# Kernel optimization log

Hardware: AMD Instinct MI355X
Metric: run time of the kernel (lower is better)

## Reference

```python
import jax, jax.numpy as jnp
import numpy as np

D_MODEL = 1024
N_HEADS = 16
SCALES = (1, 2)
D_K = D_MODEL // N_HEADS          # 64
HPS = N_HEADS // len(SCALES)      # heads per scale = 8


def _upsample_linear(x, target_len):
    """PyTorch F.interpolate(mode='linear', align_corners=False) along dim 2.
    x: [b, h, l, d] -> [b, h, target_len, d]"""
    b, h, l, d = x.shape
    if l == target_len:
        return x
    # source coordinates, clamped at 0 like PyTorch's area_pixel_compute_source_index
    coords = (jnp.arange(target_len, dtype=jnp.float32) + 0.5) * (l / target_len) - 0.5
    coords = jnp.maximum(coords, 0.0)
    i0 = jnp.clip(jnp.floor(coords).astype(jnp.int32), 0, l - 1)
    i1 = jnp.minimum(i0 + 1, l - 1)
    w = (coords - i0.astype(jnp.float32))[None, None, :, None]
    return x[:, :, i0, :] * (1.0 - w) + x[:, :, i1, :] * w


def setup_inputs() -> dict:
    rng = jax.random.key(0)
    ks = jax.random.split(rng, 7)
    B, S = 2, 2048
    s = 1.0 / np.sqrt(D_MODEL)
    mkw = lambda k: jax.random.normal(k, (D_MODEL, D_MODEL), jnp.float32) * s
    zb = jnp.zeros((D_MODEL,), jnp.float32)
    return {
        "query": jax.random.normal(ks[0], (B, S, D_MODEL), jnp.float32),
        "key": jax.random.normal(ks[1], (B, S, D_MODEL), jnp.float32),
        "value": jax.random.normal(ks[2], (B, S, D_MODEL), jnp.float32),
        "w_q": mkw(ks[3]), "b_q": zb,
        "w_k": mkw(ks[4]), "b_k": zb,
        "w_v": mkw(ks[5]), "b_v": zb,
        "w_o": mkw(ks[6]), "b_o": zb,
    }


def reference(query, key, value, w_q, b_q, w_k, b_k, w_v, b_v, w_o, b_o):
    B, S, _ = query.shape
    inv_scale = 1.0 / np.sqrt(D_K).astype(np.float32)

    def proj(x, W, b):
        # [B,S,D] -> [B,H,S,dk]
        return (x @ W + b).reshape(B, S, N_HEADS, D_K).transpose(0, 2, 1, 3)

    Q = proj(query, w_q, b_q)
    K = proj(key, w_k, b_k)
    V = proj(value, w_v, b_v)

    outs = []
    for i, f in enumerate(SCALES):
        hs = slice(i * HPS, (i + 1) * HPS)
        Qd = Q[:, hs, ::f]                      # strided downsample along seq
        Kd = K[:, hs, ::f]
        Vd = V[:, hs, ::f]
        scores = jnp.einsum('bhqd,bhkd->bhqk', Qd, Kd) * inv_scale
        attn = jax.nn.softmax(scores, axis=-1)   # dropout inactive (eval)
        o = jnp.einsum('bhqk,bhkd->bhqd', attn, Vd)
        outs.append(_upsample_linear(o, S))

    out = jnp.concatenate(outs, axis=1)          # [B,H,S,dk]
    out = out.transpose(0, 2, 1, 3).reshape(B, S, D_MODEL)
    return out @ w_o + b_o
```

## Files before the change

kernel.cpp:

```cpp
#include <hip/hip_runtime.h>
#include <hip/hip_bf16.h>
#include <cstddef>

#define DMODEL 1024
#define DK 64
#define S1 2048
#define S2 1024
#define NBATCH 2
#define NSPLIT 2
#define KVTILE 64
#define QSCALE 0.1803368801111244f

typedef __bf16 bf16x8 __attribute__((ext_vector_type(8)));
typedef float f32x4 __attribute__((ext_vector_type(4)));
typedef unsigned short u16x4 __attribute__((ext_vector_type(4)));
typedef unsigned int u32x4 __attribute__((ext_vector_type(4)));

__device__ __forceinline__ unsigned short f2bf(float f) {
  unsigned u = __builtin_bit_cast(unsigned, f);
  u = (u + 0x7FFFu + ((u >> 16) & 1u)) >> 16;
  return (unsigned short)u;
}
__device__ __forceinline__ float bf2f(unsigned short u) {
  unsigned x = ((unsigned)u) << 16;
  return __builtin_bit_cast(float, x);
}
__device__ __forceinline__ unsigned cvt_pk_bf16(float a, float b) {
  unsigned r;
  asm("v_cvt_pk_bf16_f32 %0, %1, %2" : "=v"(r) : "v"(a), "v"(b));
  return r;
}
__device__ __forceinline__ bf16x8 ld_bf16x8(const unsigned short* p) {
  u32x4 v = *reinterpret_cast<const u32x4*>(p);
  return __builtin_bit_cast(bf16x8, v);
}
__device__ __forceinline__ void gload_lds16(const void* g, void* l) {
  __builtin_amdgcn_global_load_lds(
      (const __attribute__((address_space(1))) unsigned*)g,
      (__attribute__((address_space(3))) unsigned*)l, 16, 0, 0);
}
__device__ __forceinline__ bf16x8 ld_tile(const unsigned short* tile, int row, int cbytes) {
  const char* p = (const char*)tile + row * 128 + (cbytes ^ ((row & 7) << 4));
  return ld_bf16x8((const unsigned short*)p);
}

__global__ __launch_bounds__(256) void cvt_bf16_kernel(
    const float* __restrict__ in, unsigned short* __restrict__ out, int n4) {
  int i = blockIdx.x * 256 + threadIdx.x;
  if (i >= n4) return;
  f32x4 v = reinterpret_cast<const f32x4*>(in)[i];
  u16x4 r;
#pragma unroll
  for (int j = 0; j < 4; ++j) r[j] = f2bf(v[j]);
  reinterpret_cast<u16x4*>(out)[i] = r;
}

__global__ __launch_bounds__(1024) void transpose_w_kernel(
    const float* __restrict__ W, unsigned short* __restrict__ Wt) {
  __shared__ float t[32][33];
  int tx = threadIdx.x, ty = threadIdx.y;
  int n = blockIdx.x * 32 + tx;
  int k = blockIdx.y * 32 + ty;
  t[ty][tx] = W[(size_t)k * DMODEL + n];
  __syncthreads();
  int n2 = blockIdx.x * 32 + ty;
  int k2 = blockIdx.y * 32 + tx;
  Wt[(size_t)n2 * DMODEL + k2] = f2bf(t[tx][ty]);
}

template <int MODE>
__global__ __launch_bounds__(256) void gemm_bf16(
    const unsigned short* __restrict__ A, const unsigned short* __restrict__ Bt,
    const float* __restrict__ bias, float sc, float* __restrict__ outF,
    unsigned short* __restrict__ out1, unsigned short* __restrict__ out2) {
  __shared__ __align__(16) unsigned short As[2][128 * 64];
  __shared__ __align__(16) unsigned short Bs[2][64 * 64];
  int w = threadIdx.x >> 6, lane = threadIdx.x & 63;
  int lo = lane & 15, hi = lane >> 4;
  int rowBase = blockIdx.y * 128;
  int colBase = blockIdx.x * 64;
  int rl = lane >> 3;
  int ck = lane & 7;

  auto stageA = [&](int buf, int k0) {
#pragma unroll
    for (int i = 0; i < 4; ++i) {
      int slot = w * 4 + i;
      int rloc = slot * 8 + rl;
      int cb = (ck * 16) ^ ((rloc & 7) << 4);
      const char* g = (const char*)(A + (size_t)(rowBase + rloc) * DMODEL + k0) + cb;
      gload_lds16(g, (void*)&As[buf][slot * 512]);
    }
  };
  auto stageB = [&](int buf, int k0) {
#pragma unroll
    for (int i = 0; i < 2; ++i) {
      int slot = w * 2 + i;
      int rloc = slot * 8 + rl;
      int cb = (ck * 16) ^ ((rloc & 7) << 4);
      const char* g = (const char*)(Bt + (size_t)(colBase + rloc) * DMODEL + k0) + cb;
      gload_lds16(g, (void*)&Bs[buf][slot * 512]);
    }
  };

  f32x4 acc[2][4] = {};

  stageA(0, 0);
  stageB(0, 0);
  __syncthreads();

  const int NT = DMODEL / 64;
  for (int t = 0; t < NT; ++t) {
    int buf = t & 1;
    if (t + 1 < NT) {
      stageA(buf ^ 1, (t + 1) * 64);
      stageB(buf ^ 1, (t + 1) * 64);
    }
    bf16x8 af[2][2], bfr[4][2];
#pragma unroll
    for (int mt = 0; mt < 2; ++mt)
#pragma unroll
      for (int kk = 0; kk < 2; ++kk)
        af[mt][kk] = ld_tile(&As[buf][0], w * 32 + mt * 16 + lo, kk * 64 + hi * 16);
#pragma unroll
    for (int nt = 0; nt < 4; ++nt)
#pragma unroll
      for (int kk = 0; kk < 2; ++kk)
        bfr[nt][kk] = ld_tile(&Bs[buf][0], nt * 16 + lo, kk * 64 + hi * 16);
#pragma unroll
    for (int kk = 0; kk < 2; ++kk)
#pragma unroll
      for (int mt = 0; mt < 2; ++mt)
#pragma unroll
        for (int nt = 0; nt < 4; ++nt)
          acc[mt][nt] = __builtin_amdgcn_mfma_f32_16x16x32_bf16(
              af[mt][kk], bfr[nt][kk], acc[mt][nt], 0, 0, 0);
    __syncthreads();
  }

#pragma unroll
  for (int mt = 0; mt < 2; ++mt) {
#pragma unroll
    for (int nt = 0; nt < 4; ++nt) {
      int col = colBase + nt * 16 + lo;
      float bv = bias[col];
#pragma unroll
      for (int r = 0; r < 4; ++r) {
        int row = rowBase + w * 32 + mt * 16 + hi * 4 + r;
        float v = (acc[mt][nt][r] + bv) * sc;
        if (MODE == 0) {
          outF[(size_t)row * DMODEL + col] = v;
        } else {
          int b = row >> 11, s = row & 2047;
          int h = col >> 6, d = col & 63;
          if (MODE == 1) {
            if (h < 8)
              out1[(((size_t)(b * 8 + h)) * S1 + s) * DK + d] = f2bf(v);
            else if (!(s & 1))
              out2[(((size_t)(b * 8 + (h - 8))) * S2 + (s >> 1)) * DK + d] = f2bf(v);
          } else {
            if (h < 8)
              out1[(((size_t)(b * 8 + h)) * DK + d) * S1 + s] = f2bf(v);
            else if (!(s & 1))
              out2[(((size_t)(b * 8 + (h - 8))) * DK + d) * S2 + (s >> 1)] = f2bf(v);
          }
        }
      }
    }
  }
}

__global__ __launch_bounds__(256) void attn_kernel(
    const unsigned short* __restrict__ Q, const unsigned short* __restrict__ K,
    const unsigned short* __restrict__ Vt, float* __restrict__ Opart,
    float* __restrict__ ml, int Sq, int Skv) {
  __shared__ __align__(16) unsigned short KV[2][2][64 * 64];
  __shared__ __align__(16) unsigned P_lds[4][16][36];
  int w = threadIdx.x >> 6, lane = threadIdx.x & 63;
  int lo = lane & 15, hi = lane >> 4;
  int bh = blockIdx.z;
  int split = blockIdx.y;
  int q0 = blockIdx.x * 64 + w * 16;
  int splitLen = Skv / NSPLIT;
  int kvbase = split * splitLen;
  int nIter = splitLen / KVTILE;

  const unsigned short* Qp = Q + ((size_t)bh * Sq + q0) * DK;
  bf16x8 qb0 = ld_bf16x8(Qp + lo * DK + hi * 8);
  bf16x8 qb1 = ld_bf16x8(Qp + lo * DK + 32 + hi * 8);

  const unsigned short* Kb = K + (size_t)bh * Skv * DK;
  const unsigned short* Vb = Vt + (size_t)bh * DK * Skv;

  auto stage = [&](int buf, int kv0) {
    int rl = lane >> 3;
    int cbl = (lane & 7) * 16;
#pragma unroll
    for (int i = 0; i < 2; ++i) {
      int rt = w * 16 + i * 8 + rl;
      int gcb = cbl ^ ((rt & 7) << 4);
      const char* gK = (const char*)(Kb + (size_t)(kv0 + rt) * DK) + gcb;
      gload_lds16(gK, (void*)&KV[buf][0][(w * 16 + i * 8) * 64]);
      const char* gV = (const char*)(Vb + (size_t)rt * Skv + kv0) + gcb;
      gload_lds16(gV, (void*)&KV[buf][1][(w * 16 + i * 8) * 64]);
    }
  };

  float m = -1e30f, l = 0.f;
  f32x4 oacc[4] = {};

  stage(0, kvbase);
  __syncthreads();

  for (int it = 0; it < nIter; ++it) {
    if (it + 1 < nIter) stage((it + 1) & 1, kvbase + (it + 1) * KVTILE);

    const unsigned short* Kt = &KV[it & 1][0][0];
    const unsigned short* Vtl = &KV[it & 1][1][0];

    f32x4 s[4];
#pragma unroll
    for (int t = 0; t < 4; ++t) {
      bf16x8 ka0 = ld_tile(Kt, t * 16 + lo, hi * 16);
      bf16x8 ka1 = ld_tile(Kt, t * 16 + lo, 64 + hi * 16);
      f32x4 z = {};
      z = __builtin_amdgcn_mfma_f32_16x16x32_bf16(ka0, qb0, z, 0, 0, 0);
      s[t] = __builtin_amdgcn_mfma_f32_16x16x32_bf16(ka1, qb1, z, 0, 0, 0);
    }

    float x[16];
#pragma unroll
    for (int t = 0; t < 4; ++t)
#pragma unroll
      for (int r = 0; r < 4; ++r) x[t * 4 + r] = s[t][r];
    float tmax = x[0];
#pragma unroll
    for (int j = 1; j < 16; ++j) tmax = fmaxf(tmax, x[j]);
    tmax = fmaxf(tmax, __shfl_xor(tmax, 16));
    tmax = fmaxf(tmax, __shfl_xor(tmax, 32));

    if (!__all(tmax - m <= 8.0f)) {
      float mnew = fmaxf(m, tmax);
      float alpha = exp2f(m - mnew);
      m = mnew;
      l *= alpha;
      float ar[4];
#pragma unroll
      for (int r = 0; r < 4; ++r) ar[r] = __shfl(alpha, hi * 4 + r);
#pragma unroll
      for (int nb = 0; nb < 4; ++nb) {
        f32x4 t = oacc[nb];
        t[0] *= ar[0];
        t[1] *= ar[1];
        t[2] *= ar[2];
        t[3] *= ar[3];
        oacc[nb] = t;
      }
    }

    float tsum = 0.f;
#pragma unroll
    for (int j = 0; j < 16; ++j) {
      x[j] = exp2f(x[j] - m);
      tsum += x[j];
    }
    tsum += __shfl_xor(tsum, 16);
    tsum += __shfl_xor(tsum, 32);
    l += tsum;

    unsigned* prow = &P_lds[w][lo][0];
#pragma unroll
    for (int t = 0; t < 4; ++t) {
      uint2 pk;
      pk.x = cvt_pk_bf16(x[t * 4 + 0], x[t * 4 + 1]);
      pk.y = cvt_pk_bf16(x[t * 4 + 2], x[t * 4 + 3]);
      *reinterpret_cast<uint2*>(prow + t * 8 + 2 * hi) = pk;
    }

    bf16x8 pa0 = ld_bf16x8(reinterpret_cast<unsigned short*>(prow + 4 * hi));
    bf16x8 pa1 = ld_bf16x8(reinterpret_cast<unsigned short*>(prow + 16 + 4 * hi));
#pragma unroll
    for (int nb = 0; nb < 4; ++nb) {
      bf16x8 vb0 = ld_tile(Vtl, nb * 16 + lo, hi * 16);
      bf16x8 vb1 = ld_tile(Vtl, nb * 16 + lo, 64 + hi * 16);
      oacc[nb] = __builtin_amdgcn_mfma_f32_16x16x32_bf16(pa0, vb0, oacc[nb], 0, 0, 0);
      oacc[nb] = __builtin_amdgcn_mfma_f32_16x16x32_bf16(pa1, vb1, oacc[nb], 0, 0, 0);
    }

    __syncthreads();
  }

  float* Op = Opart + (((size_t)(split * 16 + bh)) * Sq + q0) * DK;
#pragma unroll
  for (int nb = 0; nb < 4; ++nb)
#pragma unroll
    for (int r = 0; r < 4; ++r)
      Op[(size_t)(hi * 4 + r) * DK + nb * 16 + lo] = oacc[nb][r];
  if (hi == 0) {
    float2* mlp = reinterpret_cast<float2*>(ml) + ((size_t)(split * 16 + bh)) * Sq + q0 + lo;
    *mlp = make_float2(m, l);
  }
}

template <int MODE>
__global__ __launch_bounds__(256) void combine_kernel(
    const float* __restrict__ Opart, const float* __restrict__ ml,
    unsigned short* __restrict__ out, int Sq) {
  int rr = blockIdx.x * 4 + (threadIdx.x >> 6);
  int d = threadIdx.x & 63;
  int bh = rr / Sq, q = rr - bh * Sq;
  const float2* mlp = reinterpret_cast<const float2*>(ml);
  float2 ml0 = mlp[(size_t)bh * Sq + q];
  float2 ml1 = mlp[(size_t)(16 + bh) * Sq + q];
  float M = fmaxf(ml0.x, ml1.x);
  float w0 = exp2f(ml0.x - M), w1 = exp2f(ml1.x - M);
  float inv = 1.0f / (ml0.y * w0 + ml1.y * w1);
  float o0 = Opart[((size_t)bh * Sq + q) * DK + d];
  float o1 = Opart[((size_t)(16 + bh) * Sq + q) * DK + d];
  float v = (o0 * w0 + o1 * w1) * inv;
  if (MODE == 1) {
    int b = bh >> 3, h = bh & 7;
    out[((size_t)(b * S1 + q)) * DMODEL + h * 64 + d] = f2bf(v);
  } else {
    out[((size_t)bh * Sq + q) * DK + d] = f2bf(v);
  }
}

__global__ __launch_bounds__(256) void upsample_kernel(
    const unsigned short* __restrict__ O2, unsigned short* __restrict__ ctx) {
  int c = blockIdx.x * 256 + threadIdx.x;
  if (c >= NBATCH * S1 * 512) return;
  int col = c & 511;
  int m_ = c >> 9;
  int s = m_ & (S1 - 1);
  int b = m_ >> 11;
  int h = col >> 6, d = col & 63;
  const unsigned short* X = O2 + ((size_t)(b * 8 + h)) * S2 * DK + d;
  int mm = s >> 1;
  float v;
  if (s & 1) {
    int i1 = (mm + 1 < S2) ? mm + 1 : S2 - 1;
    v = 0.75f * bf2f(X[(size_t)mm * DK]) + 0.25f * bf2f(X[(size_t)i1 * DK]);
  } else {
    v = (mm == 0) ? bf2f(X[0])
                  : (0.25f * bf2f(X[(size_t)(mm - 1) * DK]) +
                     0.75f * bf2f(X[(size_t)mm * DK]));
  }
  ctx[((size_t)(b * S1 + s)) * DMODEL + 512 + col] = f2bf(v);
}

extern "C" void kernel_launch(void* const* d_in, const int* in_sizes, int n_in,
                              void* d_out, int out_size, void* d_ws, size_t ws_size,
                              hipStream_t stream) {
  const float* query = (const float*)d_in[0];
  const float* key = (const float*)d_in[1];
  const float* value = (const float*)d_in[2];
  const float* w_q = (const float*)d_in[3];
  const float* b_q = (const float*)d_in[4];
  const float* w_k = (const float*)d_in[5];
  const float* b_k = (const float*)d_in[6];
  const float* w_v = (const float*)d_in[7];
  const float* b_v = (const float*)d_in[8];
  const float* w_o = (const float*)d_in[9];
  const float* b_o = (const float*)d_in[10];
  float* out = (float*)d_out;

  char* ws = (char*)d_ws;
  size_t off = 0;
  auto alloc = [&](size_t bytes) {
    char* p = ws + off;
    off += (bytes + 255) & ~(size_t)255;
    return p;
  };
  const size_t WT_B = (size_t)DMODEL * DMODEL * 2;
  unsigned short* WqT = (unsigned short*)alloc(WT_B);
  unsigned short* WkT = (unsigned short*)alloc(WT_B);
  unsigned short* WvT = (unsigned short*)alloc(WT_B);
  unsigned short* WoT = (unsigned short*)alloc(WT_B);
  unsigned short* xk = (unsigned short*)alloc((size_t)NBATCH * S1 * DMODEL * 2);
  unsigned short* xv = (unsigned short*)alloc((size_t)NBATCH * S1 * DMODEL * 2);
  float* Opart1 = (float*)xk;
  unsigned short* Q1 = (unsigned short*)alloc((size_t)16 * S1 * DK * 2);
  unsigned short* K1 = (unsigned short*)alloc((size_t)16 * S1 * DK * 2);
  unsigned short* V1t = (unsigned short*)alloc((size_t)16 * S1 * DK * 2);
  unsigned short* Q2 = (unsigned short*)alloc((size_t)16 * S2 * DK * 2);
  unsigned short* K2 = (unsigned short*)alloc((size_t)16 * S2 * DK * 2);
  unsigned short* V2t = (unsigned short*)alloc((size_t)16 * S2 * DK * 2);
  unsigned short* O2 = (unsigned short*)alloc((size_t)16 * S2 * DK * 2);
  unsigned short* ctx = (unsigned short*)alloc((size_t)NBATCH * S1 * DMODEL * 2);
  unsigned short* xq = ctx;
  float* Opart2 = (float*)alloc((size_t)NSPLIT * 16 * S2 * DK * 4);
  float* ml1 = (float*)alloc((size_t)NSPLIT * 16 * S1 * 2 * 4);
  float* ml2 = (float*)alloc((size_t)NSPLIT * 16 * S2 * 2 * 4);

  const int n4 = NBATCH * S1 * DMODEL / 4;
  cvt_bf16_kernel<<<n4 / 256, 256, 0, stream>>>(query, xq, n4);
  cvt_bf16_kernel<<<n4 / 256, 256, 0, stream>>>(key, xk, n4);
  cvt_bf16_kernel<<<n4 / 256, 256, 0, stream>>>(value, xv, n4);

  dim3 tb(32, 32), tg(32, 32);
  transpose_w_kernel<<<tg, tb, 0, stream>>>(w_q, WqT);
  transpose_w_kernel<<<tg, tb, 0, stream>>>(w_k, WkT);
  transpose_w_kernel<<<tg, tb, 0, stream>>>(w_v, WvT);
  transpose_w_kernel<<<tg, tb, 0, stream>>>(w_o, WoT);

  dim3 gg(DMODEL / 64, (NBATCH * S1) / 128);
  gemm_bf16<1><<<gg, 256, 0, stream>>>(xq, WqT, b_q, QSCALE, nullptr, Q1, Q2);
  gemm_bf16<1><<<gg, 256, 0, stream>>>(xk, WkT, b_k, 1.0f, nullptr, K1, K2);
  gemm_bf16<2><<<gg, 256, 0, stream>>>(xv, WvT, b_v, 1.0f, nullptr, V1t, V2t);

  attn_kernel<<<dim3(S1 / 64, NSPLIT, 16), 256, 0, stream>>>(Q1, K1, V1t, Opart1, ml1, S1, S1);
  attn_kernel<<<dim3(S2 / 64, NSPLIT, 16), 256, 0, stream>>>(Q2, K2, V2t, Opart2, ml2, S2, S2);

  combine_kernel<1><<<(16 * S1) / 4, 256, 0, stream>>>(Opart1, ml1, ctx, S1);
  combine_kernel<0><<<(16 * S2) / 4, 256, 0, stream>>>(Opart2, ml2, O2, S2);

  upsample_kernel<<<(NBATCH * S1 * 512) / 256, 256, 0, stream>>>(O2, ctx);

  gemm_bf16<0><<<gg, 256, 0, stream>>>(ctx, WoT, b_o, 1.0f, out, nullptr, nullptr);
}
```

Measured before the change: 298.5 us.

## Process two 16-row query tiles per wave to reuse K/V fragments

Each wave now handles 32 query rows as two 16-row sub-tiles, so every K and V fragment read from shared memory feeds twice as many MFMAs. The block covers 128 queries and the grid is halved. LDS tile addresses are precomputed once per wave (row offset and swizzle) instead of per load. This cuts LDS traffic and global K/V staging per query, at the cost of more registers and fewer blocks, which may reduce occupancy and parallelism on the smaller scale-2 attention.

Result: no change. 296.7 us (-0.6%).

```diff
diff --git a/kernel.cpp b/kernel.cpp
--- a/kernel.cpp
+++ b/kernel.cpp
@@ -42,6 +42,9 @@
 __device__ __forceinline__ bf16x8 ld_tile(const unsigned short* tile, int row, int cbytes) {
   const char* p = (const char*)tile + row * 128 + (cbytes ^ ((row & 7) << 4));
   return ld_bf16x8((const unsigned short*)p);
+}
+__device__ __forceinline__ bf16x8 ld_off(const void* base, int byteoff) {
+  return ld_bf16x8((const unsigned short*)((const char*)base + byteoff));
 }
 
 __global__ __launch_bounds__(256) void cvt_bf16_kernel(
@@ -175,19 +178,21 @@
     const unsigned short* __restrict__ Vt, float* __restrict__ Opart,
     float* __restrict__ ml, int Sq, int Skv) {
   __shared__ __align__(16) unsigned short KV[2][2][64 * 64];
-  __shared__ __align__(16) unsigned P_lds[4][16][36];
+  __shared__ __align__(16) unsigned P_lds[4][2][16][36];
   int w = threadIdx.x >> 6, lane = threadIdx.x & 63;
   int lo = lane & 15, hi = lane >> 4;
   int bh = blockIdx.z;
   int split = blockIdx.y;
-  int q0 = blockIdx.x * 64 + w * 16;
+  int q0 = blockIdx.x * 128 + w * 32;
   int splitLen = Skv / NSPLIT;
   int kvbase = split * splitLen;
   int nIter = splitLen / KVTILE;
 
   const unsigned short* Qp = Q + ((size_t)bh * Sq + q0) * DK;
-  bf16x8 qb0 = ld_bf16x8(Qp + lo * DK + hi * 8);
-  bf16x8 qb1 = ld_bf16x8(Qp + lo * DK + 32 + hi * 8);
+  bf16x8 qA0 = ld_bf16x8(Qp + lo * DK + hi * 8);
+  bf16x8 qA1 = ld_bf16x8(Qp + lo * DK + 32 + hi * 8);
+  bf16x8 qB0 = ld_bf16x8(Qp + (16 + lo) * DK + hi * 8);
+  bf16x8 qB1 = ld_bf16x8(Qp + (16 + lo) * DK + 32 + hi * 8);
 
   const unsigned short* Kb = K + (size_t)bh * Skv * DK;
   const unsigned short* Vb = Vt + (size_t)bh * DK * Skv;
@@ -206,8 +211,13 @@
     }
   };
 
-  float m = -1e30f, l = 0.f;
-  f32x4 oacc[4] = {};
+  int rowoff = lo * 128;
+  int sw = (lo & 7) << 4;
+  int colz0 = (hi * 16) ^ sw;
+  int colz1 = (64 + hi * 16) ^ sw;
+
+  float mA = -1e30f, lA = 0.f, mB = -1e30f, lB = 0.f;
+  f32x4 oaccA[4] = {}, oaccB[4] = {};
 
   stage(0, kvbase);
   __syncthreads();
@@ -215,90 +225,108 @@
   for (int it = 0; it < nIter; ++it) {
     if (it + 1 < nIter) stage((it + 1) & 1, kvbase + (it + 1) * KVTILE);
 
-    const unsigned short* Kt = &KV[it & 1][0][0];
-    const unsigned short* Vtl = &KV[it & 1][1][0];
-
-    f32x4 s[4];
+    const char* Kt = (const char*)&KV[it & 1][0][0];
+    const char* Vtl = (const char*)&KV[it & 1][1][0];
+
+    f32x4 sA[4], sB[4];
 #pragma unroll
     for (int t = 0; t < 4; ++t) {
-      bf16x8 ka0 = ld_tile(Kt, t * 16 + lo, hi * 16);
-      bf16x8 ka1 = ld_tile(Kt, t * 16 + lo, 64 + hi * 16);
-      f32x4 z = {};
-      z = __builtin_amdgcn_mfma_f32_16x16x32_bf16(ka0, qb0, z, 0, 0, 0);
-      s[t] = __builtin_amdgcn_mfma_f32_16x16x32_bf16(ka1, qb1, z, 0, 0, 0);
-    }
-
-    float x[16];
-#pragma unroll
-    for (int t = 0; t < 4; ++t)
-#pragma unroll
-      for (int r = 0; r < 4; ++r) x[t * 4 + r] = s[t][r];
-    float tmax = x[0];
-#pragma unroll
-    for (int j = 1; j < 16; ++j) tmax = fmaxf(tmax, x[j]);
-    tmax = fmaxf(tmax, __shfl_xor(tmax, 16));
-    tmax = fmaxf(tmax, __shfl_xor(tmax, 32));
-
-    if (!__all(tmax - m <= 8.0f)) {
-      float mnew = fmaxf(m, tmax);
-      float alpha = exp2f(m - mnew);
-      m = mnew;
-      l *= alpha;
-      float ar[4];
-#pragma unroll
-      for (int r = 0; r < 4; ++r) ar[r] = __shfl(alpha, hi * 4 + r);
-#pragma unroll
-      for (int nb = 0; nb < 4; ++nb) {
-        f32x4 t = oacc[nb];
-        t[0] *= ar[0];
-        t[1] *= ar[1];
-        t[2] *= ar[2];
-        t[3] *= ar[3];
-        oacc[nb] = t;
+      bf16x8 ka0 = ld_off(Kt, t * 2048 + rowoff + colz0);
+      bf16x8 ka1 = ld_off(Kt, t * 2048 + rowoff + colz1);
+      f32x4 zA = {};
+      zA = __builtin_amdgcn_mfma_f32_16x16x32_bf16(ka0, qA0, zA, 0, 0, 0);
+      sA[t] = __builtin_amdgcn_mfma_f32_16x16x32_bf16(ka1, qA1, zA, 0, 0, 0);
+      f32x4 zB = {};
+      zB = __builtin_amdgcn_mfma_f32_16x16x32_bf16(ka0, qB0, zB, 0, 0, 0);
+      sB[t] = __builtin_amdgcn_mfma_f32_16x16x32_bf16(ka1, qB1, zB, 0, 0, 0);
+    }
+
+#pragma unroll
+    for (int tile = 0; tile < 2; ++tile) {
+      f32x4* s = tile ? sB : sA;
+      float& m = tile ? mB : mA;
+      float& l = tile ? lB : lA;
+      f32x4* oacc = tile ? oaccB : oaccA;
+
+      float t01 = fmaxf(fmaxf(s[0][0], s[0][1]), fmaxf(s[0][2], s[0][3]));
+      float t23 = fmaxf(fmaxf(s[1][0], s[1][1]), fmaxf(s[1][2], s[1][3]));
+      float t45 = fmaxf(fmaxf(s[2][0], s[2][1]), fmaxf(s[2][2], s[2][3]));
+      float t67 = fmaxf(fmaxf(s[3][0], s[3][1]), fmaxf(s[3][2], s[3][3]));
+      float tmax = fmaxf(fmaxf(t01, t23), fmaxf(t45, t67));
+      tmax = fmaxf(tmax, __shfl_xor(tmax, 16));
+      tmax = fmaxf(tmax, __shfl_xor(tmax, 32));
+
+      if (!__all(tmax - m <= 8.0f)) {
+        float mnew = fmaxf(m, tmax);
+        float alpha = exp2f(m - mnew);
+        m = mnew;
+        l *= alpha;
+        float ar[4];
+#pragma unroll
+        for (int r = 0; r < 4; ++r) ar[r] = __shfl(alpha, hi * 4 + r);
+#pragma unroll
+        for (int nb = 0; nb < 4; ++nb) {
+          f32x4 t = oacc[nb];
+          t[0] *= ar[0];
+          t[1] *= ar[1];
+          t[2] *= ar[2];
+          t[3] *= ar[3];
+          oacc[nb] = t;
+        }
       }
-    }
-
-    float tsum = 0.f;
-#pragma unroll
-    for (int j = 0; j < 16; ++j) {
-      x[j] = exp2f(x[j] - m);
-      tsum += x[j];
-    }
-    tsum += __shfl_xor(tsum, 16);
-    tsum += __shfl_xor(tsum, 32);
-    l += tsum;
-
-    unsigned* prow = &P_lds[w][lo][0];
-#pragma unroll
-    for (int t = 0; t < 4; ++t) {
-      uint2 pk;
-      pk.x = cvt_pk_bf16(x[t * 4 + 0], x[t * 4 + 1]);
-      pk.y = cvt_pk_bf16(x[t * 4 + 2], x[t * 4 + 3]);
-      *reinterpret_cast<uint2*>(prow + t * 8 + 2 * hi) = pk;
-    }
-
-    bf16x8 pa0 = ld_bf16x8(reinterpret_cast<unsigned short*>(prow + 4 * hi));
-    bf16x8 pa1 = ld_bf16x8(reinterpret_cast<unsigned short*>(prow + 16 + 4 * hi));
+
+      float tsum = 0.f;
+#pragma unroll
+      for (int t = 0; t < 4; ++t)
+#pragma unroll
+        for (int r = 0; r < 4; ++r) {
+          s[t][r] = exp2f(s[t][r] - m);
+          tsum += s[t][r];
+        }
+      tsum += __shfl_xor(tsum, 16);
+      tsum += __shfl_xor(tsum, 32);
+      l += tsum;
+
+      unsigned* prow = &P_lds[w][tile][lo][0];
+#pragma unroll
+      for (int t = 0; t < 4; ++t) {
+        uint2 pk;
+        pk.x = cvt_pk_bf16(s[t][0], s[t][1]);
+        pk.y = cvt_pk_bf16(s[t][2], s[t][3]);
+        *reinterpret_cast<uint2*>(prow + t * 8 + 2 * hi) = pk;
+      }
+    }
+
+    bf16x8 paA0 = ld_bf16x8((unsigned short*)(&P_lds[w][0][lo][0] + 4 * hi));
+    bf16x8 paA1 = ld_bf16x8((unsigned short*)(&P_lds[w][0][lo][0] + 16 + 4 * hi));
+    bf16x8 paB0 = ld_bf16x8((unsigned short*)(&P_lds[w][1][lo][0] + 4 * hi));
+    bf16x8 paB1 = ld_bf16x8((unsigned short*)(&P_lds[w][1][lo][0] + 16 + 4 * hi));
 #pragma unroll
     for (int nb = 0; nb < 4; ++nb) {
-      bf16x8 vb0 = ld_tile(Vtl, nb * 16 + lo, hi * 16);
-      bf16x8 vb1 = ld_tile(Vtl, nb * 16 + lo, 64 + hi * 16);
-      oacc[nb] = __builtin_amdgcn_mfma_f32_16x16x32_bf16(pa0, vb0, oacc[nb], 0, 0, 0);
-      oacc[nb] = __builtin_amdgcn_mfma_f32_16x16x32_bf16(pa1, vb1, oacc[nb], 0, 0, 0);
+      bf16x8 vb0 = ld_off(Vtl, nb * 2048 + rowoff + colz0);
+      bf16x8 vb1 = ld_off(Vtl, nb * 2048 + rowoff + colz1);
+      oaccA[nb] = __builtin_amdgcn_mfma_f32_16x16x32_bf16(paA0, vb0, oaccA[nb], 0, 0, 0);
+      oaccA[nb] = __builtin_amdgcn_mfma_f32_16x16x32_bf16(paA1, vb1, oaccA[nb], 0, 0, 0);
+      oaccB[nb] = __builtin_amdgcn_mfma_f32_16x16x32_bf16(paB0, vb0, oaccB[nb], 0, 0, 0);
+      oaccB[nb] = __builtin_amdgcn_mfma_f32_16x16x32_bf16(paB1, vb1, oaccB[nb], 0, 0, 0);
     }
 
     __syncthreads();
   }
 
-  float* Op = Opart + (((size_t)(split * 16 + bh)) * Sq + q0) * DK;
+  float* OpA = Opart + (((size_t)(split * 16 + bh)) * Sq + q0) * DK;
+  float* OpB = OpA + (size_t)16 * DK;
 #pragma unroll
   for (int nb = 0; nb < 4; ++nb)
 #pragma unroll
-    for (int r = 0; r < 4; ++r)
-      Op[(size_t)(hi * 4 + r) * DK + nb * 16 + lo] = oacc[nb][r];
+    for (int r = 0; r < 4; ++r) {
+      OpA[(size_t)(hi * 4 + r) * DK + nb * 16 + lo] = oaccA[nb][r];
+      OpB[(size_t)(hi * 4 + r) * DK + nb * 16 + lo] = oaccB[nb][r];
+    }
   if (hi == 0) {
     float2* mlp = reinterpret_cast<float2*>(ml) + ((size_t)(split * 16 + bh)) * Sq + q0 + lo;
-    *mlp = make_float2(m, l);
+    mlp[0] = make_float2(mA, lA);
+    mlp[16] = make_float2(mB, lB);
   }
 }
 
@@ -409,8 +437,8 @@
   gemm_bf16<1><<<gg, 256, 0, stream>>>(xk, WkT, b_k, 1.0f, nullptr, K1, K2);
   gemm_bf16<2><<<gg, 256, 0, stream>>>(xv, WvT, b_v, 1.0f, nullptr, V1t, V2t);
 
-  attn_kernel<<<dim3(S1 / 64, NSPLIT, 16), 256, 0, stream>>>(Q1, K1, V1t, Opart1, ml1, S1, S1);
-  attn_kernel<<<dim3(S2 / 64, NSPLIT, 16), 256, 0, stream>>>(Q2, K2, V2t, Opart2, ml2, S2, S2);
+  attn_kernel<<<dim3(S1 / 128, NSPLIT, 16), 256, 0, stream>>>(Q1, K1, V1t, Opart1, ml1, S1, S1);
+  attn_kernel<<<dim3(S2 / 128, NSPLIT, 16), 256, 0, stream>>>(Q2, K2, V2t, Opart2, ml2, S2, S2);
 
   combine_kernel<1><<<(16 * S1) / 4, 256, 0, stream>>>(Opart1, ml1, ctx, S1);
   combine_kernel<0><<<(16 * S2) / 4, 256, 0, stream>>>(Opart2, ml2, O2, S2);
```
